# Performance work log

Measured on AMD Instinct MI355X. Metric: run time of the kernel, lower is better.

The kernel has to match this reference:

```python
import jax, jax.numpy as jnp
import numpy as np

NUM_HEADS = 32
NUM_KV_GROUPS = 8
HEAD_DIM = 64  # dim_out // num_heads
DIM_IN = 2048
DIM_OUT = 2048


def setup_inputs() -> dict:
    key = jax.random.key(0)
    k_x, k_q, k_k, k_v, k_o = jax.random.split(key, 5)
    s = 0.02
    x = jax.random.normal(k_x, (1, 2048, DIM_IN), dtype=jnp.float32)
    wq = jax.random.normal(k_q, (DIM_IN, DIM_OUT), dtype=jnp.float32) * s
    wk = jax.random.normal(k_k, (DIM_IN, NUM_KV_GROUPS * HEAD_DIM), dtype=jnp.float32) * s
    wv = jax.random.normal(k_v, (DIM_IN, NUM_KV_GROUPS * HEAD_DIM), dtype=jnp.float32) * s
    wo = jax.random.normal(k_o, (DIM_OUT, DIM_OUT), dtype=jnp.float32) * s
    return {"x": x, "wq": wq, "wk": wk, "wv": wv, "wo": wo}


def reference(x, wq, wk, wv, wo):
    b, n, _ = x.shape
    g, r, d = NUM_KV_GROUPS, NUM_HEADS // NUM_KV_GROUPS, HEAD_DIM
    # projections
    q = (x @ wq).reshape(b, n, g, r, d)          # [b,n,g,r,d] heads grouped
    k = (x @ wk).reshape(b, n, g, d)             # [b,n,g,d]
    v = (x @ wv).reshape(b, n, g, d)
    # scores: repeat_interleave of K over group dim == broadcast over r
    scores = jnp.einsum('bqgrd,bkgd->bgrqk', q, k)  # [b,g,r,n,n]
    causal = jnp.tril(jnp.ones((n, n), dtype=bool))
    scores = jnp.where(causal, scores, -jnp.inf)
    attn = jax.nn.softmax(scores / jnp.sqrt(jnp.asarray(d, x.dtype)), axis=-1)
    ctx = jnp.einsum('bgrqk,bkgd->bqgrd', attn, v)  # [b,n,g,r,d]
    out = ctx.reshape(b, n, g * r * d) @ wo
    return out
```

## Files before the change

kernel.cpp:

```cpp
#include <hip/hip_runtime.h>


typedef __attribute__((ext_vector_type(8))) short bf16x8;
typedef __attribute__((ext_vector_type(4))) short bf16x4;
typedef __attribute__((ext_vector_type(4))) float f32x4;

__device__ __forceinline__ short f2bf(float f) {
  unsigned u = __builtin_bit_cast(unsigned, f);
  u += 0x7FFFu + ((u >> 16) & 1u);
  return (short)(u >> 16);
}

__device__ __forceinline__ unsigned pkbf(float a, float b) {
  const unsigned ua = __builtin_bit_cast(unsigned, a) + 0x8000u;
  const unsigned ub = __builtin_bit_cast(unsigned, b) + 0x8000u;
  return __builtin_amdgcn_perm(ub, ua, 0x07060302u);
}

__device__ __forceinline__ void gload_lds16(const void* g, void* l) {
  __builtin_amdgcn_global_load_lds(
      (const __attribute__((address_space(1))) unsigned int*)g,
      (__attribute__((address_space(3))) unsigned int*)l, 16, 0, 0);
}

__global__ __launch_bounds__(256) void cvtx(const float* __restrict__ x,
                                            short* __restrict__ y) {
  const int i = (blockIdx.x * 256 + threadIdx.x) * 4;
  const float4 v = *(const float4*)&x[i];
  bf16x4 r;
  r[0] = f2bf(v.x); r[1] = f2bf(v.y); r[2] = f2bf(v.z); r[3] = f2bf(v.w);
  *(bf16x4*)&y[i] = r;
}

__global__ __launch_bounds__(256) void tcvt4(const float* __restrict__ wq,
                                             const float* __restrict__ wk,
                                             const float* __restrict__ wv,
                                             const float* __restrict__ wo,
                                             short* __restrict__ dq,
                                             short* __restrict__ dk,
                                             short* __restrict__ dv,
                                             short* __restrict__ dwo) {
  const int z = blockIdx.z;
  const float* src;
  short* dst;
  int C;
  if (z == 0)      { src = wq; dst = dq;  C = 2048; }
  else if (z == 1) { src = wk; dst = dk;  C = 512; }
  else if (z == 2) { src = wv; dst = dv;  C = 512; }
  else             { src = wo; dst = dwo; C = 2048; }
  const int c0 = blockIdx.x * 32;
  if (c0 >= C) return;
  const int R = 2048;
  __shared__ float t[32][33];
  const int r0 = blockIdx.y * 32;
  const int tx = threadIdx.x & 31, ty = threadIdx.x >> 5;
#pragma unroll
  for (int i = 0; i < 4; ++i)
    t[ty + i * 8][tx] = src[(r0 + ty + i * 8) * C + c0 + tx];
  __syncthreads();
#pragma unroll
  for (int i = 0; i < 4; ++i)
    dst[(c0 + ty + i * 8) * R + r0 + tx] = f2bf(t[tx][ty + i * 8]);
}

__global__ __launch_bounds__(256) void tbf(const short* __restrict__ src,
                                           short* __restrict__ dst,
                                           int R, int C, int ldsrc) {
  __shared__ short t[32][33];
  const int c0 = blockIdx.x * 32, r0 = blockIdx.y * 32;
  const int tx = threadIdx.x & 31, ty = threadIdx.x >> 5;
#pragma unroll
  for (int i = 0; i < 4; ++i)
    t[ty + i * 8][tx] = src[(r0 + ty + i * 8) * ldsrc + c0 + tx];
  __syncthreads();
#pragma unroll
  for (int i = 0; i < 4; ++i)
    dst[(c0 + ty + i * 8) * R + r0 + tx] = t[tx][ty + i * 8];
}

template <int OUT_BF16, int BN>
__global__ __launch_bounds__(128) void gemm_bt(const short* __restrict__ A,
                                               const short* __restrict__ B,
                                               void* __restrict__ Cv,
                                               int M, int N, int K,
                                               float cscale, int scale_cols) {
  __shared__ short As[2][64 * 64];
  __shared__ short Bs[2][BN * 64];
  const int tid = threadIdx.x;
  const int lane = tid & 63, wid = tid >> 6;
  const int l15 = lane & 15, lg = lane >> 4;
  const int lr = lane >> 3, lc = lane & 7;
  const int row0 = blockIdx.y * 64, col0 = blockIdx.x * BN;
  const int sswz = l15 & 7;
  f32x4 acc[4][BN / 32] = {};
  const int arow = wid * 8 + lr;
  const short* ag = A + (row0 + arow) * K + (lc ^ lr) * 8;
  const short* bg = B + (col0 + arow) * K + (lc ^ lr) * 8;

  auto stage = [&](int b, int kk) {
    short* lA = &As[b][wid * 512];
    short* lB = &Bs[b][wid * 512];
#pragma unroll
    for (int c = 0; c < 4; ++c)
      gload_lds16(ag + c * 16 * K + kk, lA + c * 1024);
#pragma unroll
    for (int c = 0; c < BN / 16; ++c)
      gload_lds16(bg + c * 16 * K + kk, lB + c * 1024);
  };

  stage(0, 0);
  __syncthreads();
  const int nb = K / 64;
  int buf = 0;
  for (int t = 0; t < nb; ++t) {
    if (t + 1 < nb) stage(buf ^ 1, (t + 1) * 64);
#pragma unroll
    for (int x = 0; x < 2; ++x) {
      bf16x8 af[4], bfr[BN / 32];
#pragma unroll
      for (int m = 0; m < 4; ++m)
        af[m] = *(const bf16x8*)&As[buf][(m * 16 + l15) * 64 + (((x * 4 + lg) ^ sswz) * 8)];
#pragma unroll
      for (int n = 0; n < BN / 32; ++n)
        bfr[n] = *(const bf16x8*)&Bs[buf][(wid * (BN / 2) + n * 16 + l15) * 64 + (((x * 4 + lg) ^ sswz) * 8)];
#pragma unroll
      for (int m = 0; m < 4; ++m)
#pragma unroll
        for (int n = 0; n < BN / 32; ++n)
          acc[m][n] = __builtin_amdgcn_mfma_f32_16x16x32_bf16(af[m], bfr[n],
                                                              acc[m][n], 0, 0, 0);
    }
    __syncthreads();
    buf ^= 1;
  }
#pragma unroll
  for (int m = 0; m < 4; ++m)
#pragma unroll
    for (int n = 0; n < BN / 32; ++n)
#pragma unroll
      for (int i = 0; i < 4; ++i) {
        const int r = row0 + m * 16 + lg * 4 + i;
        const int c = col0 + wid * (BN / 2) + n * 16 + l15;
        float v = acc[m][n][i];
        if (c < scale_cols) v *= cscale;
        if (OUT_BF16)
          ((short*)Cv)[r * N + c] = f2bf(v);
        else
          ((float*)Cv)[r * N + c] = v;
      }
}

__global__ __launch_bounds__(256) void attn_fwd(const short* __restrict__ QKV,
                                                const short* __restrict__ Vt,
                                                short* __restrict__ CTX) {
  const int ldq = 3072;
  const int qb = 31 - (int)blockIdx.x;
  const int h = blockIdx.y;
  const int g = h >> 2;
  const int lane = threadIdx.x & 63, wid = threadIdx.x >> 6;
  const int l15 = lane & 15, lg = lane >> 4;
  const int qrow0 = qb * 64 + wid * 16;

  __shared__ short Ks[2][64 * 64];
  __shared__ short Vs[2][64 * 64];
  __shared__ short Ps[4][16 * 64];

  const int swz = (l15 & 7) << 3;

  bf16x8 qf[2];
#pragma unroll
  for (int kc = 0; kc < 2; ++kc)
    qf[kc] = *(const bf16x8*)&QKV[(qrow0 + l15) * ldq + h * 64 + kc * 32 + lg * 8];

  float l_run = 0.f;
  f32x4 accO[4] = {};

  const int srow = threadIdx.x >> 3, sseg = threadIdx.x & 7;
  const int ssw = (sseg ^ (srow & 7)) * 8;
  const short* Kg = QKV + 2048 + g * 64 + sseg * 8;
  const short* Vg = Vt + (g * 64 + srow) * 2048 + sseg * 8;

  bf16x8 rk0 = *(const bf16x8*)&Kg[srow * ldq];
  bf16x8 rk1 = *(const bf16x8*)&Kg[(srow + 32) * ldq];
  bf16x8 rv0 = *(const bf16x8*)&Vg[0];
  bf16x8 rv1 = *(const bf16x8*)&Vg[32 * 2048];

  for (int kt = 0; kt <= qb; ++kt) {
    const int buf = kt & 1;
    const int tokbase = kt * 64;
    *(bf16x8*)&Ks[buf][srow * 64 + ssw] = rk0;
    *(bf16x8*)&Ks[buf][(srow + 32) * 64 + ssw] = rk1;
    *(bf16x8*)&Vs[buf][srow * 64 + ssw] = rv0;
    *(bf16x8*)&Vs[buf][(srow + 32) * 64 + ssw] = rv1;
    if (kt < qb) {
      const int nb = (kt + 1) * 64;
      rk0 = *(const bf16x8*)&Kg[(nb + srow) * ldq];
      rk1 = *(const bf16x8*)&Kg[(nb + srow + 32) * ldq];
      rv0 = *(const bf16x8*)&Vg[nb];
      rv1 = *(const bf16x8*)&Vg[32 * 2048 + nb];
    }
    __syncthreads();

    f32x4 s[4];
    __builtin_amdgcn_s_setprio(1);
#pragma unroll
    for (int t = 0; t < 4; ++t) {
      s[t] = (f32x4){0.f, 0.f, 0.f, 0.f};
#pragma unroll
      for (int kc = 0; kc < 2; ++kc) {
        const bf16x8 kf =
            *(const bf16x8*)&Ks[buf][(t * 16 + l15) * 64 + (((kc * 4 + lg) ^ (l15 & 7)) * 8)];
        s[t] = __builtin_amdgcn_mfma_f32_16x16x32_bf16(kf, qf[kc], s[t], 0, 0, 0);
      }
    }
    __builtin_amdgcn_s_setprio(0);

    if (kt == qb) {
      const int kq = tokbase + lg * 4 - qrow0 - l15;
#pragma unroll
      for (int t = 0; t < 4; ++t)
#pragma unroll
        for (int i = 0; i < 4; ++i)
          if (kq + t * 16 + i > 0) s[t][i] = -3e38f;
    }

    float ts[4];
#pragma unroll
    for (int t = 0; t < 4; ++t) {
      const float e0 = __builtin_amdgcn_exp2f(s[t][0]);
      const float e1 = __builtin_amdgcn_exp2f(s[t][1]);
      const float e2 = __builtin_amdgcn_exp2f(s[t][2]);
      const float e3 = __builtin_amdgcn_exp2f(s[t][3]);
      s[t][0] = e0; s[t][1] = e1; s[t][2] = e2; s[t][3] = e3;
      ts[t] = (e0 + e1) + (e2 + e3);
    }
    float rs = (ts[0] + ts[1]) + (ts[2] + ts[3]);
    rs += __shfl_xor(rs, 16);
    rs += __shfl_xor(rs, 32);
    l_run += rs;

#pragma unroll
    for (int t = 0; t < 4; ++t) {
      uint2 w;
      w.x = pkbf(s[t][0], s[t][1]);
      w.y = pkbf(s[t][2], s[t][3]);
      *(uint2*)&Ps[wid][l15 * 64 + ((t * 16 + lg * 4) ^ swz)] = w;
    }
    __builtin_amdgcn_s_setprio(1);
#pragma unroll
    for (int kc = 0; kc < 2; ++kc) {
      const bf16x8 pb =
          *(const bf16x8*)&Ps[wid][l15 * 64 + ((kc * 32 + lg * 8) ^ swz)];
#pragma unroll
      for (int t2 = 0; t2 < 4; ++t2) {
        const bf16x8 vb =
            *(const bf16x8*)&Vs[buf][(t2 * 16 + l15) * 64 + (((kc * 4 + lg) ^ (l15 & 7)) * 8)];
        accO[t2] = __builtin_amdgcn_mfma_f32_16x16x32_bf16(vb, pb, accO[t2], 0, 0, 0);
      }
    }
    __builtin_amdgcn_s_setprio(0);
  }

  const float inv = 1.0f / l_run;
#pragma unroll
  for (int t2 = 0; t2 < 4; ++t2) {
    bf16x4 w;
#pragma unroll
    for (int i = 0; i < 4; ++i) w[i] = f2bf(accO[t2][i] * inv);
    *(bf16x4*)&Ps[wid][l15 * 64 + ((t2 * 16 + lg * 4) ^ swz)] = w;
  }
#pragma unroll
  for (int r = 0; r < 2; ++r) {
    const int seg = lg + r * 4;
    const bf16x8 row = *(const bf16x8*)&Ps[wid][l15 * 64 + ((seg * 8) ^ swz)];
    *(bf16x8*)&CTX[(qrow0 + l15) * 2048 + h * 64 + seg * 8] = row;
  }
}

extern "C" void kernel_launch(void* const* d_in, const int* in_sizes, int n_in,
                              void* d_out, int out_size, void* d_ws, size_t ws_size,
                              hipStream_t stream) {
  (void)in_sizes; (void)n_in; (void)out_size; (void)ws_size;
  const float* x  = (const float*)d_in[0];
  const float* wq = (const float*)d_in[1];
  const float* wk = (const float*)d_in[2];
  const float* wv = (const float*)d_in[3];
  const float* wo = (const float*)d_in[4];
  float* out = (float*)d_out;

  char* ws = (char*)d_ws;
  short* Xb  = (short*)(ws);
  short* WT  = (short*)(ws + 8388608);
  short* WoT = (short*)(ws + 20971520);
  short* QKV = (short*)(ws + 29360128);
  short* Vt  = (short*)(ws + 41943040);
  short* CTX = (short*)(ws + 44040192);

  const float qscale = 0.125f * 1.4426950408889634f;

  cvtx<<<4096, 256, 0, stream>>>(x, Xb);
  { dim3 g(64, 64, 4);
    tcvt4<<<g, 256, 0, stream>>>(wq, wk, wv, wo,
                                 WT, WT + 2048 * 2048, WT + 2560 * 2048, WoT); }
  { dim3 g(24, 32); gemm_bt<1, 128><<<g, 128, 0, stream>>>(Xb, WT, QKV, 2048, 3072, 2048, qscale, 2048); }
  { dim3 g(16, 64); tbf<<<g, 256, 0, stream>>>(QKV + 2560, Vt, 2048, 512, 3072); }
  { dim3 g(32, 32); attn_fwd<<<g, 256, 0, stream>>>(QKV, Vt, CTX); }
  { dim3 g(32, 32); gemm_bt<0, 64><<<g, 128, 0, stream>>>(CTX, WoT, out, 2048, 2048, 2048, 1.0f, 0); }
}
```

Before: 143.3 us.

## Process two query heads per attention block sharing K/V tiles; retile QKV GEMM

The attention kernel now handles two heads of the same KV group per workgroup, so each loaded K/V tile feeds MFMAs for both heads and the grid's y dimension is halved. This cuts repeated K/V global loads and LDS staging per head, but doubles the accumulator and score registers and the P buffer in LDS, which may lower occupancy. Separately, the QKV projection GEMM switches from 128-wide to 96-wide column tiles with a larger grid, which changes the wave count and load balance.

```diff
diff --git a/kernel.cpp b/kernel.cpp
--- a/kernel.cpp
+++ b/kernel.cpp
@@ -155,25 +155,28 @@
                                                 short* __restrict__ CTX) {
   const int ldq = 3072;
   const int qb = 31 - (int)blockIdx.x;
-  const int h = blockIdx.y;
-  const int g = h >> 2;
+  const int hp = blockIdx.y;
+  const int g = hp >> 1;
+  const int h0 = g * 4 + (hp & 1) * 2;
   const int lane = threadIdx.x & 63, wid = threadIdx.x >> 6;
   const int l15 = lane & 15, lg = lane >> 4;
   const int qrow0 = qb * 64 + wid * 16;
 
   __shared__ short Ks[2][64 * 64];
   __shared__ short Vs[2][64 * 64];
-  __shared__ short Ps[4][16 * 64];
+  __shared__ short Ps[4][2][16 * 64];
 
   const int swz = (l15 & 7) << 3;
 
-  bf16x8 qf[2];
-#pragma unroll
-  for (int kc = 0; kc < 2; ++kc)
-    qf[kc] = *(const bf16x8*)&QKV[(qrow0 + l15) * ldq + h * 64 + kc * 32 + lg * 8];
-
-  float l_run = 0.f;
-  f32x4 accO[4] = {};
+  bf16x8 qf[2][2];
+#pragma unroll
+  for (int hh = 0; hh < 2; ++hh)
+#pragma unroll
+    for (int kc = 0; kc < 2; ++kc)
+      qf[hh][kc] = *(const bf16x8*)&QKV[(qrow0 + l15) * ldq + (h0 + hh) * 64 + kc * 32 + lg * 8];
+
+  float l_run[2] = {0.f, 0.f};
+  f32x4 accO[2][4] = {};
 
   const int srow = threadIdx.x >> 3, sseg = threadIdx.x & 7;
   const int ssw = (sseg ^ (srow & 7)) * 8;
@@ -201,16 +204,18 @@
     }
     __syncthreads();
 
-    f32x4 s[4];
+    f32x4 s[2][4];
     __builtin_amdgcn_s_setprio(1);
 #pragma unroll
     for (int t = 0; t < 4; ++t) {
-      s[t] = (f32x4){0.f, 0.f, 0.f, 0.f};
+      s[0][t] = (f32x4){0.f, 0.f, 0.f, 0.f};
+      s[1][t] = (f32x4){0.f, 0.f, 0.f, 0.f};
 #pragma unroll
       for (int kc = 0; kc < 2; ++kc) {
         const bf16x8 kf =
             *(const bf16x8*)&Ks[buf][(t * 16 + l15) * 64 + (((kc * 4 + lg) ^ (l15 & 7)) * 8)];
-        s[t] = __builtin_amdgcn_mfma_f32_16x16x32_bf16(kf, qf[kc], s[t], 0, 0, 0);
+        s[0][t] = __builtin_amdgcn_mfma_f32_16x16x32_bf16(kf, qf[0][kc], s[0][t], 0, 0, 0);
+        s[1][t] = __builtin_amdgcn_mfma_f32_16x16x32_bf16(kf, qf[1][kc], s[1][t], 0, 0, 0);
       }
     }
     __builtin_amdgcn_s_setprio(0);
@@ -221,59 +226,69 @@
       for (int t = 0; t < 4; ++t)
 #pragma unroll
         for (int i = 0; i < 4; ++i)
-          if (kq + t * 16 + i > 0) s[t][i] = -3e38f;
-    }
-
-    float ts[4];
+          if (kq + t * 16 + i > 0) { s[0][t][i] = -3e38f; s[1][t][i] = -3e38f; }
+    }
+
+#pragma unroll
+    for (int hh = 0; hh < 2; ++hh) {
+      float ts[4];
+#pragma unroll
+      for (int t = 0; t < 4; ++t) {
+        const float e0 = __builtin_amdgcn_exp2f(s[hh][t][0]);
+        const float e1 = __builtin_amdgcn_exp2f(s[hh][t][1]);
+        const float e2 = __builtin_amdgcn_exp2f(s[hh][t][2]);
+        const float e3 = __builtin_amdgcn_exp2f(s[hh][t][3]);
+        s[hh][t][0] = e0; s[hh][t][1] = e1; s[hh][t][2] = e2; s[hh][t][3] = e3;
+        ts[t] = (e0 + e1) + (e2 + e3);
+      }
+      float rs = (ts[0] + ts[1]) + (ts[2] + ts[3]);
+      rs += __shfl_xor(rs, 16);
+      rs += __shfl_xor(rs, 32);
+      l_run[hh] += rs;
+    }
+
 #pragma unroll
     for (int t = 0; t < 4; ++t) {
-      const float e0 = __builtin_amdgcn_exp2f(s[t][0]);
-      const float e1 = __builtin_amdgcn_exp2f(s[t][1]);
-      const float e2 = __builtin_amdgcn_exp2f(s[t][2]);
-      const float e3 = __builtin_amdgcn_exp2f(s[t][3]);
-      s[t][0] = e0; s[t][1] = e1; s[t][2] = e2; s[t][3] = e3;
-      ts[t] = (e0 + e1) + (e2 + e3);
-    }
-    float rs = (ts[0] + ts[1]) + (ts[2] + ts[3]);
-    rs += __shfl_xor(rs, 16);
-    rs += __shfl_xor(rs, 32);
-    l_run += rs;
-
-#pragma unroll
-    for (int t = 0; t < 4; ++t) {
-      uint2 w;
-      w.x = pkbf(s[t][0], s[t][1]);
-      w.y = pkbf(s[t][2], s[t][3]);
-      *(uint2*)&Ps[wid][l15 * 64 + ((t * 16 + lg * 4) ^ swz)] = w;
+      uint2 w0, w1;
+      w0.x = pkbf(s[0][t][0], s[0][t][1]); w0.y = pkbf(s[0][t][2], s[0][t][3]);
+      w1.x = pkbf(s[1][t][0], s[1][t][1]); w1.y = pkbf(s[1][t][2], s[1][t][3]);
+      *(uint2*)&Ps[wid][0][l15 * 64 + ((t * 16 + lg * 4) ^ swz)] = w0;
+      *(uint2*)&Ps[wid][1][l15 * 64 + ((t * 16 + lg * 4) ^ swz)] = w1;
     }
     __builtin_amdgcn_s_setprio(1);
 #pragma unroll
     for (int kc = 0; kc < 2; ++kc) {
-      const bf16x8 pb =
-          *(const bf16x8*)&Ps[wid][l15 * 64 + ((kc * 32 + lg * 8) ^ swz)];
+      const bf16x8 pb0 =
+          *(const bf16x8*)&Ps[wid][0][l15 * 64 + ((kc * 32 + lg * 8) ^ swz)];
+      const bf16x8 pb1 =
+          *(const bf16x8*)&Ps[wid][1][l15 * 64 + ((kc * 32 + lg * 8) ^ swz)];
 #pragma unroll
       for (int t2 = 0; t2 < 4; ++t2) {
         const bf16x8 vb =
             *(const bf16x8*)&Vs[buf][(t2 * 16 + l15) * 64 + (((kc * 4 + lg) ^ (l15 & 7)) * 8)];
-        accO[t2] = __builtin_amdgcn_mfma_f32_16x16x32_bf16(vb, pb, accO[t2], 0, 0, 0);
+        accO[0][t2] = __builtin_amdgcn_mfma_f32_16x16x32_bf16(vb, pb0, accO[0][t2], 0, 0, 0);
+        accO[1][t2] = __builtin_amdgcn_mfma_f32_16x16x32_bf16(vb, pb1, accO[1][t2], 0, 0, 0);
       }
     }
     __builtin_amdgcn_s_setprio(0);
   }
 
-  const float inv = 1.0f / l_run;
-#pragma unroll
-  for (int t2 = 0; t2 < 4; ++t2) {
-    bf16x4 w;
-#pragma unroll
-    for (int i = 0; i < 4; ++i) w[i] = f2bf(accO[t2][i] * inv);
-    *(bf16x4*)&Ps[wid][l15 * 64 + ((t2 * 16 + lg * 4) ^ swz)] = w;
-  }
-#pragma unroll
-  for (int r = 0; r < 2; ++r) {
-    const int seg = lg + r * 4;
-    const bf16x8 row = *(const bf16x8*)&Ps[wid][l15 * 64 + ((seg * 8) ^ swz)];
-    *(bf16x8*)&CTX[(qrow0 + l15) * 2048 + h * 64 + seg * 8] = row;
+#pragma unroll
+  for (int hh = 0; hh < 2; ++hh) {
+    const float inv = 1.0f / l_run[hh];
+#pragma unroll
+    for (int t2 = 0; t2 < 4; ++t2) {
+      bf16x4 w;
+#pragma unroll
+      for (int i = 0; i < 4; ++i) w[i] = f2bf(accO[hh][t2][i] * inv);
+      *(bf16x4*)&Ps[wid][hh][l15 * 64 + ((t2 * 16 + lg * 4) ^ swz)] = w;
+    }
+#pragma unroll
+    for (int r = 0; r < 2; ++r) {
+      const int seg = lg + r * 4;
+      const bf16x8 row = *(const bf16x8*)&Ps[wid][hh][l15 * 64 + ((seg * 8) ^ swz)];
+      *(bf16x8*)&CTX[(qrow0 + l15) * 2048 + (h0 + hh) * 64 + seg * 8] = row;
+    }
   }
 }
 
@@ -302,8 +317,8 @@
   { dim3 g(64, 64, 4);
     tcvt4<<<g, 256, 0, stream>>>(wq, wk, wv, wo,
                                  WT, WT + 2048 * 2048, WT + 2560 * 2048, WoT); }
-  { dim3 g(24, 32); gemm_bt<1, 128><<<g, 128, 0, stream>>>(Xb, WT, QKV, 2048, 3072, 2048, qscale, 2048); }
+  { dim3 g(32, 32); gemm_bt<1, 96><<<g, 128, 0, stream>>>(Xb, WT, QKV, 2048, 3072, 2048, qscale, 2048); }
   { dim3 g(16, 64); tbf<<<g, 256, 0, stream>>>(QKV + 2560, Vt, 2048, 512, 3072); }
-  { dim3 g(32, 32); attn_fwd<<<g, 256, 0, stream>>>(QKV, Vt, CTX); }
+  { dim3 g(32, 16); attn_fwd<<<g, 256, 0, stream>>>(QKV, Vt, CTX); }
   { dim3 g(32, 32); gemm_bt<0, 64><<<g, 128, 0, stream>>>(CTX, WoT, out, 2048, 2048, 2048, 1.0f, 0); }
 }
```

Result: faster. 134.0 us (-6.5%).
